# Kernel tuning notes

Measured on AMD Instinct MI355X. Metric: run time of the kernel, lower is better.

The kernel has to match this reference:

```python
import jax, jax.numpy as jnp
import numpy as np

# Reversible solver constants (init kwargs / solve args)
L = 0.999          # coupling parameter l
H = 1.0 / 64.0     # step size h
T_END = 1.0        # terminal time T
N_STEPS = int(T_END / H)  # 64 sequential steps

B, D, HID = 4096, 512, 2048


def setup_inputs() -> dict:
    key = jax.random.key(0)
    k0, k1, k2, k3 = jax.random.split(key, 4)
    s1 = 1.0 / np.sqrt(D).astype(np.float32)
    s2 = 1.0 / np.sqrt(HID).astype(np.float32)
    return {
        "y0": jax.random.normal(k0, (B, D), jnp.float32),
        "W1": jax.random.normal(k1, (D, HID), jnp.float32) * s1,
        "b1": jnp.zeros((HID,), jnp.float32),
        "wt": jax.random.normal(k2, (HID,), jnp.float32) * 0.1,
        "W2": jax.random.normal(k3, (HID, D), jnp.float32) * s2,
        "b2": jnp.zeros((D,), jnp.float32),
    }


def reference(y0, W1, b1, wt, W2, b2):
    # MLP vector field vf(t, y): [B, D] -> [B, D]
    def vf(t, y):
        hidden = jnp.tanh(y @ W1 + b1 + t * wt)  # [B, HID]
        return hidden @ W2 + b2                   # [B, D]

    # Explicit Euler solver step: step(vf, h, t, y) = h * vf(t, y)
    def euler_step(hh, t, y):
        return hh * vf(t, y)

    # Reversible forward step (faithful to _solve_forward.forward_step)
    def forward_step(carry, _):
        t0, y0_, z0 = carry
        t1 = t0 + H
        y1 = L * y0_ + (1.0 - L) * z0 + euler_step(H, t0, z0)
        z1 = z0 - euler_step(-H, t1, y1)
        return (t1, y1, z1), None

    t0 = jnp.zeros((), jnp.float32)
    (tN, yN, zN), _ = jax.lax.scan(forward_step, (t0, y0, y0), None, length=N_STEPS)
    return yN
```

## Files before the change

kernel.cpp:

```cpp
#include <hip/hip_runtime.h>
#include <hip/hip_bf16.h>

typedef __bf16 bf16x8 __attribute__((ext_vector_type(8)));
typedef float f32x4 __attribute__((ext_vector_type(4)));
typedef unsigned short u16;

#define GLD_LDS16(gp, lp) __builtin_amdgcn_global_load_lds( \
    (const __attribute__((address_space(1))) unsigned int*)(gp), \
    (__attribute__((address_space(3))) unsigned int*)(lp), 16, 0, 0)

__device__ __forceinline__ float tanh_fast(float x) {
  float e = __expf(2.0f * x);
  return 1.0f - __fdividef(2.0f, e + 1.0f);
}

__device__ __forceinline__ u16 bf16_rn(float x) {
  union { float f; unsigned u; } v; v.f = x;
  unsigned r = v.u + 0x7fffu + ((v.u >> 16) & 1u);
  return (u16)(r >> 16);
}

template <int BM, int BN, int BK, int K, int MODE, int NTL>
__global__ __launch_bounds__(256)
void gemm_fused(const u16* __restrict__ A, const u16* __restrict__ Bt,
                const float* __restrict__ bias, const float* __restrict__ wt,
                float tval,
                const float* __restrict__ y_in, const float* __restrict__ z_in,
                float* __restrict__ out32, u16* __restrict__ out_bf, int N) {
  constexpr int NS = BK / 64;
  constexpr int WTM = BM / 2, WTN = BN / 2;
  constexpr int FM = WTM / 16, FN = WTN / 16;
  constexpr int ACH = BM * BK * 2 / 1024;
  constexpr int BCH = BN * BK * 2 / 1024;
  constexpr int CPS_A = BM / 8;
  constexpr int CPS_B = BN / 8;
  constexpr int MT = 4096 / BM;
  constexpr int MPX = MT / 8;

  __shared__ u16 As[NS * BM * 64];
  __shared__ u16 Bs[NS * BN * 64];

  const int tid = threadIdx.x;
  const int wave = tid >> 6;
  const int lane = tid & 63;
  const int wm = wave >> 1, wn = wave & 1;
  const int l15 = lane & 15, kg = lane >> 4;

  const int wg = blockIdx.x;
  const int xcd = wg & 7;
  const int j = wg >> 3;
  const int bm0 = (xcd * MPX + j / NTL) * BM;
  const int bn0 = (j % NTL) * BN;

  f32x4 acc[FM][FN];
#pragma unroll
  for (int m = 0; m < FM; ++m)
#pragma unroll
    for (int n = 0; n < FN; ++n) acc[m][n] = (f32x4){0.f, 0.f, 0.f, 0.f};

  const int sr = lane >> 3;
  const int scs = ((lane & 7) ^ sr) * 8;
  const int rsw = (l15 & 7) << 3;

  const u16* Ag = A + (size_t)bm0 * K;
  const u16* Bg = Bt + (size_t)bn0 * K;

  for (int kt = 0; kt < K / BK; ++kt) {
    const u16* Ak = Ag + kt * BK;
    const u16* Bk = Bg + kt * BK;
#pragma unroll
    for (int i = 0; i < ACH / 4; ++i) {
      const int ch = wave + i * 4;
      const int kh = ch / CPS_A;
      const int rg = ch % CPS_A;
      GLD_LDS16(Ak + (size_t)(rg * 8 + sr) * K + kh * 64 + scs,
                (char*)As + ch * 1024);
    }
#pragma unroll
    for (int i = 0; i < BCH / 4; ++i) {
      const int ch = wave + i * 4;
      const int kh = ch / CPS_B;
      const int rg = ch % CPS_B;
      GLD_LDS16(Bk + (size_t)(rg * 8 + sr) * K + kh * 64 + scs,
                (char*)Bs + ch * 1024);
    }
    __syncthreads();
#pragma unroll
    for (int ks = 0; ks < 2 * NS; ++ks) {
      const int kh = ks >> 1;
      const int kc = ((ks & 1) * 32 + kg * 8) ^ rsw;
      bf16x8 af[FM], bfr[FN];
#pragma unroll
      for (int m = 0; m < FM; ++m)
        af[m] = *reinterpret_cast<const bf16x8*>(
            &As[(kh * BM + wm * WTM + m * 16 + l15) * 64 + kc]);
#pragma unroll
      for (int n = 0; n < FN; ++n)
        bfr[n] = *reinterpret_cast<const bf16x8*>(
            &Bs[(kh * BN + wn * WTN + n * 16 + l15) * 64 + kc]);
#pragma unroll
      for (int m = 0; m < FM; ++m)
#pragma unroll
        for (int n = 0; n < FN; ++n)
          acc[m][n] =
              __builtin_amdgcn_mfma_f32_16x16x32_bf16(af[m], bfr[n], acc[m][n], 0, 0, 0);
    }
    __syncthreads();
  }

#pragma unroll
  for (int n = 0; n < FN; ++n) {
    const int col = bn0 + wn * WTN + n * 16 + l15;
    const float bv = bias[col];
    const float wv = (MODE == 0) ? wt[col] : 0.f;
#pragma unroll
    for (int m = 0; m < FM; ++m) {
      const int row0 = bm0 + wm * WTM + m * 16 + kg * 4;
#pragma unroll
      for (int r = 0; r < 4; ++r) {
        const size_t idx = (size_t)(row0 + r) * N + col;
        const float a = acc[m][n][r];
        if (MODE == 0) {
          const float x = a + bv + tval * wv;
          out_bf[idx] = bf16_rn(tanh_fast(x));
        } else if (MODE == 1) {
          const float v = 0.999f * y_in[idx] + 0.001f * z_in[idx] +
                          0.015625f * (a + bv);
          out32[idx] = v;
          out_bf[idx] = bf16_rn(v);
        } else {
          const float v = z_in[idx] + 0.015625f * (a + bv);
          out32[idx] = v;
          out_bf[idx] = bf16_rn(v);
        }
      }
    }
  }
}

__global__ void transpose_bf16(const float* __restrict__ in, u16* __restrict__ out,
                               int R, int C) {
  __shared__ float tile[32][33];
  const int bx = blockIdx.x * 32;
  const int by = blockIdx.y * 32;
  const int tx = threadIdx.x, ty = threadIdx.y;
#pragma unroll
  for (int i = 0; i < 32; i += 8)
    tile[ty + i][tx] = in[(size_t)(by + ty + i) * C + (bx + tx)];
  __syncthreads();
#pragma unroll
  for (int i = 0; i < 32; i += 8)
    out[(size_t)(bx + ty + i) * R + (by + tx)] = bf16_rn(tile[tx][ty + i]);
}

__global__ void init_state(const float* __restrict__ y0, float* __restrict__ y32,
                           float* __restrict__ z32, u16* __restrict__ zbf, int n) {
  const int i = blockIdx.x * blockDim.x + threadIdx.x;
  if (i < n) {
    const float v = y0[i];
    y32[i] = v;
    z32[i] = v;
    zbf[i] = bf16_rn(v);
  }
}

extern "C" void kernel_launch(void* const* d_in, const int* in_sizes, int n_in,
                              void* d_out, int out_size, void* d_ws, size_t ws_size,
                              hipStream_t stream) {
  const float* y0 = (const float*)d_in[0];
  const float* W1 = (const float*)d_in[1];
  const float* b1 = (const float*)d_in[2];
  const float* wt = (const float*)d_in[3];
  const float* W2 = (const float*)d_in[4];
  const float* b2 = (const float*)d_in[5];

  constexpr int B = 4096, D = 512, HID = 2048, NSTEP = 64;
  constexpr float Hh = 1.0f / 64.0f;

  char* ws = (char*)d_ws;
  u16* W1t = (u16*)ws; ws += (size_t)HID * D * 2;
  u16* W2t = (u16*)ws; ws += (size_t)D * HID * 2;
  u16* hid = (u16*)ws; ws += (size_t)B * HID * 2;
  float* z32 = (float*)ws; ws += (size_t)B * D * 4;
  u16* ybf = (u16*)ws; ws += (size_t)B * D * 2;
  u16* zbf = (u16*)ws; ws += (size_t)B * D * 2;
  float* y32 = (float*)d_out;

  transpose_bf16<<<dim3(HID / 32, D / 32), dim3(32, 8), 0, stream>>>(W1, W1t, D, HID);
  transpose_bf16<<<dim3(D / 32, HID / 32), dim3(32, 8), 0, stream>>>(W2, W2t, HID, D);
  init_state<<<(B * D + 255) / 256, 256, 0, stream>>>(y0, y32, z32, zbf, B * D);

  for (int s = 0; s < NSTEP; ++s) {
    const float t0 = (float)s * Hh;
    const float t1 = (float)(s + 1) * Hh;
    gemm_fused<64, 128, 128, 512, 0, 16><<<1024, 256, 0, stream>>>(
        zbf, W1t, b1, wt, t0, nullptr, nullptr, nullptr, hid, HID);
    gemm_fused<32, 64, 256, 2048, 1, 8><<<1024, 256, 0, stream>>>(
        hid, W2t, b2, nullptr, 0.f, y32, z32, y32, ybf, D);
    gemm_fused<64, 128, 128, 512, 0, 16><<<1024, 256, 0, stream>>>(
        ybf, W1t, b1, wt, t1, nullptr, nullptr, nullptr, hid, HID);
    gemm_fused<32, 64, 256, 2048, 2, 8><<<1024, 256, 0, stream>>>(
        hid, W2t, b2, nullptr, 0.f, nullptr, z32, z32, zbf, D);
  }
}
```

Baseline: 5.172 ms.

## Split GEMMs into hidden and update kernels with intra-block split-K reduction

The first GEMM (W1) moves to larger 128x128 tiles with 512 blocks. The second GEMM (W2, K=2048) gets its own kernel using 64x64 tiles in which each wave takes a different k-slice of every BK chunk. The partial sums are reduced through LDS, and the epilogue then does vectorized float4 loads and stores of the y/z state. This aims at better MFMA operand reuse and coalesced epilogue memory traffic, at the cost of an LDS reduction pass and fewer blocks per launch.

Measured after the change: 4.548 ms. -12.1%, faster.

```diff
diff --git a/kernel.cpp b/kernel.cpp
--- a/kernel.cpp
+++ b/kernel.cpp
@@ -20,13 +20,11 @@
   return (u16)(r >> 16);
 }
 
-template <int BM, int BN, int BK, int K, int MODE, int NTL>
+template <int BM, int BN, int BK, int K, int NTL>
 __global__ __launch_bounds__(256)
-void gemm_fused(const u16* __restrict__ A, const u16* __restrict__ Bt,
-                const float* __restrict__ bias, const float* __restrict__ wt,
-                float tval,
-                const float* __restrict__ y_in, const float* __restrict__ z_in,
-                float* __restrict__ out32, u16* __restrict__ out_bf, int N) {
+void gemm_hidden(const u16* __restrict__ A, const u16* __restrict__ Bt,
+                 const float* __restrict__ bias, const float* __restrict__ wt,
+                 float tval, u16* __restrict__ out_bf, int N) {
   constexpr int NS = BK / 64;
   constexpr int WTM = BM / 2, WTN = BN / 2;
   constexpr int FM = WTM / 16, FN = WTN / 16;
@@ -111,30 +109,146 @@
 #pragma unroll
   for (int n = 0; n < FN; ++n) {
     const int col = bn0 + wn * WTN + n * 16 + l15;
-    const float bv = bias[col];
-    const float wv = (MODE == 0) ? wt[col] : 0.f;
+    const float bv = bias[col] + tval * wt[col];
 #pragma unroll
     for (int m = 0; m < FM; ++m) {
       const int row0 = bm0 + wm * WTM + m * 16 + kg * 4;
 #pragma unroll
-      for (int r = 0; r < 4; ++r) {
-        const size_t idx = (size_t)(row0 + r) * N + col;
-        const float a = acc[m][n][r];
-        if (MODE == 0) {
-          const float x = a + bv + tval * wv;
-          out_bf[idx] = bf16_rn(tanh_fast(x));
-        } else if (MODE == 1) {
-          const float v = 0.999f * y_in[idx] + 0.001f * z_in[idx] +
-                          0.015625f * (a + bv);
-          out32[idx] = v;
-          out_bf[idx] = bf16_rn(v);
-        } else {
-          const float v = z_in[idx] + 0.015625f * (a + bv);
-          out32[idx] = v;
-          out_bf[idx] = bf16_rn(v);
-        }
+      for (int r = 0; r < 4; ++r)
+        out_bf[(size_t)(row0 + r) * N + col] = bf16_rn(tanh_fast(acc[m][n][r] + bv));
+    }
+  }
+}
+
+template <int MODE>
+__global__ __launch_bounds__(256)
+void gemm_update(const u16* __restrict__ A, const u16* __restrict__ Bt,
+                 const float* __restrict__ bias,
+                 const float* __restrict__ y_in, const float* __restrict__ z_in,
+                 float* __restrict__ out32, u16* __restrict__ out_bf) {
+  constexpr int BM = 64, BN = 64, BK = 256, K = 2048, N = 512, NTL = 8;
+  constexpr int NS = BK / 64;
+  constexpr int NT = K / BK;
+  constexpr int CPS = BM / 8;
+  constexpr int MPX = (4096 / BM) / 8;
+
+  __shared__ __align__(16) char smem[64 * 1024];
+  u16* As = (u16*)smem;
+  u16* Bs = (u16*)(smem + 32 * 1024);
+  float* red = (float*)smem;
+
+  const int tid = threadIdx.x;
+  const int wave = tid >> 6;
+  const int lane = tid & 63;
+  const int l15 = lane & 15, kg = lane >> 4;
+
+  const int wg = blockIdx.x;
+  const int xcd = wg & 7;
+  const int j = wg >> 3;
+  const int bm0 = (xcd * MPX + j / NTL) * BM;
+  const int bn0 = (j % NTL) * BN;
+
+  f32x4 acc[4][4];
+#pragma unroll
+  for (int m = 0; m < 4; ++m)
+#pragma unroll
+    for (int n = 0; n < 4; ++n) acc[m][n] = (f32x4){0.f, 0.f, 0.f, 0.f};
+
+  const int sr = lane >> 3;
+  const int scs = ((lane & 7) ^ sr) * 8;
+  const int rsw = (l15 & 7) << 3;
+
+  const u16* Ag = A + (size_t)bm0 * K;
+  const u16* Bg = Bt + (size_t)bn0 * K;
+
+  for (int kt = 0; kt < NT; ++kt) {
+    const u16* Ak = Ag + kt * BK;
+    const u16* Bk = Bg + kt * BK;
+#pragma unroll
+    for (int i = 0; i < 8; ++i) {
+      const int ch = wave + i * 4;
+      const int kh = ch / CPS;
+      const int rg = ch % CPS;
+      GLD_LDS16(Ak + (size_t)(rg * 8 + sr) * K + kh * 64 + scs,
+                (char*)As + ch * 1024);
+    }
+#pragma unroll
+    for (int i = 0; i < 8; ++i) {
+      const int ch = wave + i * 4;
+      const int kh = ch / CPS;
+      const int rg = ch % CPS;
+      GLD_LDS16(Bk + (size_t)(rg * 8 + sr) * K + kh * 64 + scs,
+                (char*)Bs + ch * 1024);
+    }
+    __syncthreads();
+#pragma unroll
+    for (int ks2 = 0; ks2 < 2; ++ks2) {
+      const int ks = wave * 2 + ks2;
+      const int kh = ks >> 1;
+      const int kc = ((ks & 1) * 32 + kg * 8) ^ rsw;
+      bf16x8 af[4], bfr[4];
+#pragma unroll
+      for (int m = 0; m < 4; ++m)
+        af[m] = *reinterpret_cast<const bf16x8*>(
+            &As[(kh * BM + m * 16 + l15) * 64 + kc]);
+#pragma unroll
+      for (int n = 0; n < 4; ++n)
+        bfr[n] = *reinterpret_cast<const bf16x8*>(
+            &Bs[(kh * BN + n * 16 + l15) * 64 + kc]);
+#pragma unroll
+      for (int m = 0; m < 4; ++m)
+#pragma unroll
+        for (int n = 0; n < 4; ++n)
+          acc[m][n] =
+              __builtin_amdgcn_mfma_f32_16x16x32_bf16(af[m], bfr[n], acc[m][n], 0, 0, 0);
+    }
+    __syncthreads();
+  }
+
+  {
+    float* my = red + wave * 4096;
+#pragma unroll
+    for (int m = 0; m < 4; ++m)
+#pragma unroll
+      for (int n = 0; n < 4; ++n)
+#pragma unroll
+        for (int r = 0; r < 4; ++r)
+          my[(m * 16 + kg * 4 + r) * 64 + n * 16 + l15] = acc[m][n][r];
+  }
+  __syncthreads();
+
+  const int row = tid >> 2;
+  const int cq = (tid & 3) * 16;
+  const size_t gbase = (size_t)(bm0 + row) * N + bn0 + cq;
+#pragma unroll
+  for (int i = 0; i < 4; ++i) {
+    const int lidx = row * 64 + cq + i * 4;
+    const f32x4 p0 = *reinterpret_cast<const f32x4*>(&red[lidx]);
+    const f32x4 p1 = *reinterpret_cast<const f32x4*>(&red[4096 + lidx]);
+    const f32x4 p2 = *reinterpret_cast<const f32x4*>(&red[8192 + lidx]);
+    const f32x4 p3 = *reinterpret_cast<const f32x4*>(&red[12288 + lidx]);
+    const f32x4 bv = *reinterpret_cast<const f32x4*>(&bias[bn0 + cq + i * 4]);
+    const f32x4 z4 = *reinterpret_cast<const f32x4*>(&z_in[gbase + i * 4]);
+    f32x4 v;
+    if (MODE == 1) {
+      const f32x4 y4 = *reinterpret_cast<const f32x4*>(&y_in[gbase + i * 4]);
+#pragma unroll
+      for (int q = 0; q < 4; ++q) {
+        const float s = ((p0[q] + p1[q]) + (p2[q] + p3[q])) + bv[q];
+        v[q] = 0.999f * y4[q] + 0.001f * z4[q] + 0.015625f * s;
       }
-    }
+    } else {
+#pragma unroll
+      for (int q = 0; q < 4; ++q) {
+        const float s = ((p0[q] + p1[q]) + (p2[q] + p3[q])) + bv[q];
+        v[q] = z4[q] + 0.015625f * s;
+      }
+    }
+    *reinterpret_cast<f32x4*>(&out32[gbase + i * 4]) = v;
+    ushort4 pb;
+    pb.x = bf16_rn(v[0]); pb.y = bf16_rn(v[1]);
+    pb.z = bf16_rn(v[2]); pb.w = bf16_rn(v[3]);
+    *reinterpret_cast<ushort4*>(&out_bf[gbase + i * 4]) = pb;
   }
 }
 
@@ -193,13 +307,11 @@
   for (int s = 0; s < NSTEP; ++s) {
     const float t0 = (float)s * Hh;
     const float t1 = (float)(s + 1) * Hh;
-    gemm_fused<64, 128, 128, 512, 0, 16><<<1024, 256, 0, stream>>>(
-        zbf, W1t, b1, wt, t0, nullptr, nullptr, nullptr, hid, HID);
-    gemm_fused<32, 64, 256, 2048, 1, 8><<<1024, 256, 0, stream>>>(
-        hid, W2t, b2, nullptr, 0.f, y32, z32, y32, ybf, D);
-    gemm_fused<64, 128, 128, 512, 0, 16><<<1024, 256, 0, stream>>>(
-        ybf, W1t, b1, wt, t1, nullptr, nullptr, nullptr, hid, HID);
-    gemm_fused<32, 64, 256, 2048, 2, 8><<<1024, 256, 0, stream>>>(
-        hid, W2t, b2, nullptr, 0.f, nullptr, z32, z32, zbf, D);
-  }
-}
+    gemm_hidden<128, 128, 128, 512, 16><<<512, 256, 0, stream>>>(
+        zbf, W1t, b1, wt, t0, hid, HID);
+    gemm_update<1><<<512, 256, 0, stream>>>(hid, W2t, b2, y32, z32, y32, ybf);
+    gemm_hidden<128, 128, 128, 512, 16><<<512, 256, 0, stream>>>(
+        ybf, W1t, b1, wt, t1, hid, HID);
+    gemm_update<2><<<512, 256, 0, stream>>>(hid, W2t, b2, nullptr, z32, z32, zbf);
+  }
+}
```
